# Kernel tuning notes

Measured on AMD Instinct MI355X. Metric: run time of the kernel, lower is better.

## Reference

```python
import jax, jax.numpy as jnp
import numpy as np

N_NODES = 50000
N_EDGES = 800000
D = 256
N_LAYERS = 2


def setup_inputs() -> dict:
    key = jax.random.key(0)
    k1, k2, k3, k4, k5, k6 = jax.random.split(key, 6)
    inp = {}
    inp["input"] = jax.random.normal(k1, (N_NODES, D), dtype=jnp.float32)
    inp["edge_index"] = jax.random.randint(k2, (2, N_EDGES), 0, N_NODES, dtype=jnp.int64)
    # learned params: initial dense projection + per-conv GCN weights
    scale = 1.0 / np.sqrt(D)
    inp["weight"] = jax.random.normal(k3, (D, D), dtype=jnp.float32) * scale
    inp["bias"] = jnp.zeros((D,), dtype=jnp.float32)
    inp["conv_w"] = jax.random.normal(k4, (N_LAYERS, D, D), dtype=jnp.float32) * scale
    inp["conv_b"] = jnp.zeros((N_LAYERS, D), dtype=jnp.float32)
    return inp


def _gcn_conv(x, W, b, src, dst, n):
    # Standard GCNConv: x' = D^{-1/2} (A + I) D^{-1/2} (x W) + b
    h = x @ W  # [N, D]
    loops = jnp.arange(n, dtype=src.dtype)
    s = jnp.concatenate([src, loops])
    d = jnp.concatenate([dst, loops])
    deg = jax.ops.segment_sum(jnp.ones(s.shape[0], dtype=x.dtype), d, num_segments=n)
    dinv = jnp.where(deg > 0, deg ** -0.5, 0.0)
    norm = dinv[s] * dinv[d]  # [E+N]
    msg = h[s] * norm[:, None]  # gather + scale  [E+N, D]
    return jax.ops.segment_sum(msg, d, num_segments=n) + b  # scatter-add


def reference(input, edge_index, weight, bias, conv_w, conv_b):
    n = input.shape[0]
    src, dst = edge_index[0], edge_index[1]
    # dropout=0 / eval mode -> identity
    x = jax.nn.relu(input @ weight + bias)
    for i in range(conv_w.shape[0]):
        x = jax.nn.relu(_gcn_conv(x, conv_w[i], conv_b[i], src, dst, n))
    return x
```

## Files before the change

### kernel.cpp

```cpp
#include <hip/hip_runtime.h>

#define D 256
typedef unsigned short u16;
typedef __attribute__((ext_vector_type(8))) short bf16x8;
typedef __attribute__((ext_vector_type(4))) float f32x4;

__device__ __forceinline__ float bf2f(u16 u) {
    union { unsigned int i; float f; } x; x.i = ((unsigned int)u) << 16; return x.f;
}
__device__ __forceinline__ u16 f2bf(float f) {
    union { float f; unsigned int i; } x; x.f = f;
    unsigned int r = x.i + 0x7fff + ((x.i >> 16) & 1);
    return (u16)(r >> 16);
}
__device__ __forceinline__ void gload16(const void* g, void* l) {
    __builtin_amdgcn_global_load_lds(
        (const __attribute__((address_space(1))) void*)g,
        (__attribute__((address_space(3))) void*)l, 16, 0, 0);
}


__global__ void init_kernel(int* __restrict__ deg, int* __restrict__ cursor, int n) {
    int i = blockIdx.x * blockDim.x + threadIdx.x;
    if (i < n) { deg[i] = 1; cursor[i] = 0; }
}

__global__ void hist_kernel(const int* __restrict__ dst, int* __restrict__ deg, int e) {
    int i = blockIdx.x * blockDim.x + threadIdx.x;
    int b = i * 4;
    if (b + 3 < e) {
        int4 v = *reinterpret_cast<const int4*>(&dst[b]);
        atomicAdd(&deg[v.x], 1); atomicAdd(&deg[v.y], 1);
        atomicAdd(&deg[v.z], 1); atomicAdd(&deg[v.w], 1);
    } else {
        for (int j = b; j < e; ++j) atomicAdd(&deg[dst[j]], 1);
    }
}

__global__ void dinv_kernel(const int* __restrict__ deg, float* __restrict__ dinv, int n) {
    int i = blockIdx.x * blockDim.x + threadIdx.x;
    if (i < n) dinv[i] = rsqrtf((float)deg[i]);
}


__global__ __launch_bounds__(256) void scan_phase1(
    const int* __restrict__ deg, int* __restrict__ bsum, int n) {
    __shared__ int red[256];
    int t = threadIdx.x;
    int i0 = blockIdx.x * 1024 + t * 4;
    int s = 0;
    if (i0 + 3 < n) {
        int4 v = *reinterpret_cast<const int4*>(&deg[i0]);
        s = v.x + v.y + v.z + v.w - 4;
    } else {
        for (int j = i0; j < n && j < i0 + 4; ++j) s += deg[j] - 1;
    }
    red[t] = s;
    __syncthreads();
    for (int off = 128; off > 0; off >>= 1) {
        if (t < off) red[t] += red[t + off];
        __syncthreads();
    }
    if (t == 0) bsum[blockIdx.x] = red[0];
}

__global__ __launch_bounds__(256) void scan_phase2(
    const int* __restrict__ bsum, int* __restrict__ boff,
    int* __restrict__ rowptr, int nblk, int n) {
    __shared__ int sums[256];
    int t = threadIdx.x;
    int v = (t < nblk) ? bsum[t] : 0;
    int orig = v;
    sums[t] = v;
    __syncthreads();
    for (int off = 1; off < 256; off <<= 1) {
        int u = (t >= off) ? sums[t - off] : 0;
        __syncthreads();
        sums[t] += u;
        __syncthreads();
    }
    if (t < nblk) boff[t] = sums[t] - orig;
    if (t == nblk - 1) rowptr[n] = sums[t];
}

__global__ __launch_bounds__(256) void scan_phase3(
    const int* __restrict__ deg, const int* __restrict__ boff,
    int* __restrict__ rowptr, int n) {
    __shared__ int sums[256];
    int t = threadIdx.x;
    int i0 = blockIdx.x * 1024 + t * 4;
    int d0 = 0, d1 = 0, d2 = 0, d3 = 0;
    if (i0 + 3 < n) {
        int4 v = *reinterpret_cast<const int4*>(&deg[i0]);
        d0 = v.x - 1; d1 = v.y - 1; d2 = v.z - 1; d3 = v.w - 1;
    } else {
        if (i0 + 0 < n) d0 = deg[i0 + 0] - 1;
        if (i0 + 1 < n) d1 = deg[i0 + 1] - 1;
        if (i0 + 2 < n) d2 = deg[i0 + 2] - 1;
        if (i0 + 3 < n) d3 = deg[i0 + 3] - 1;
    }
    int ts = d0 + d1 + d2 + d3;
    sums[t] = ts;
    __syncthreads();
    for (int off = 1; off < 256; off <<= 1) {
        int u = (t >= off) ? sums[t - off] : 0;
        __syncthreads();
        sums[t] += u;
        __syncthreads();
    }
    int pre = boff[blockIdx.x] + sums[t] - ts;
    if (i0 + 0 < n) rowptr[i0 + 0] = pre; pre += d0;
    if (i0 + 1 < n) rowptr[i0 + 1] = pre; pre += d1;
    if (i0 + 2 < n) rowptr[i0 + 2] = pre; pre += d2;
    if (i0 + 3 < n) rowptr[i0 + 3] = pre;
}

__global__ void fill_kernel(const int* __restrict__ src, const int* __restrict__ dst,
                            const int* __restrict__ rowptr, int* __restrict__ cursor,
                            int* __restrict__ csr, int e) {
    int i = blockIdx.x * blockDim.x + threadIdx.x;
    if (i < e) {
        int d = dst[i];
        int p = atomicAdd(&cursor[d], 1);
        csr[rowptr[d] + p] = src[i];
    }
}


__global__ void cvt_kernel(const float* __restrict__ in, u16* __restrict__ out, int n4) {
    int i = blockIdx.x * blockDim.x + threadIdx.x;
    if (i < n4) {
        float4 v = *reinterpret_cast<const float4*>(&in[(size_t)i * 4]);
        ushort4 o;
        o.x = f2bf(v.x); o.y = f2bf(v.y); o.z = f2bf(v.z); o.w = f2bf(v.w);
        *reinterpret_cast<ushort4*>(&out[(size_t)i * 4]) = o;
    }
}

__global__ __launch_bounds__(256) void transpose_cvt_kernel(
    const float* __restrict__ W, u16* __restrict__ Wt) {
    __shared__ float t[32][33];
    int bx = blockIdx.x * 32, by = blockIdx.y * 32;
    int tx = threadIdx.x & 31, ty = threadIdx.x >> 5;
#pragma unroll
    for (int i = 0; i < 32; i += 8)
        t[ty + i][tx] = W[(size_t)(bx + ty + i) * D + by + tx];
    __syncthreads();
#pragma unroll
    for (int i = 0; i < 32; i += 8)
        Wt[(size_t)(by + ty + i) * D + bx + tx] = f2bf(t[tx][ty + i]);
}

__global__ __launch_bounds__(256) void mfma_gemm(
    const u16* __restrict__ A, const u16* __restrict__ Bt,
    const float* __restrict__ bias, const float* __restrict__ dinv,
    u16* __restrict__ C, int M, int mode)
{
    __shared__ u16 As[128 * 32];
    __shared__ u16 Bs[128 * 32];
    const int tid = threadIdx.x;
    const int lane = tid & 63;
    const int wave = tid >> 6;
    const int wr = wave >> 1, wc = wave & 1;
    const int row0 = blockIdx.y * 128, col0 = blockIdx.x * 128;
    const int l16 = lane & 15, kg = lane >> 4;

    f32x4 acc[4][4] = {};

    for (int k0 = 0; k0 < D; k0 += 32) {
#pragma unroll
        for (int i = 0; i < 2; ++i) {
            int idx = i * 256 + tid;
            int r = idx >> 2, c = idx & 3;
            int csw = c ^ ((r >> 1) & 3);
            char* ldsbase_a = (char*)As + ((i * 256 + (tid & ~63)) << 4);
            char* ldsbase_b = (char*)Bs + ((i * 256 + (tid & ~63)) << 4);
            int grow = row0 + r; if (grow >= M) grow = M - 1;
            gload16(&A[(size_t)grow * D + k0 + csw * 8], ldsbase_a);
            gload16(&Bt[(size_t)(col0 + r) * D + k0 + csw * 8], ldsbase_b);
        }
        __syncthreads();
        bf16x8 af[4], bfr[4];
        int ksw = kg ^ ((l16 >> 1) & 3);
#pragma unroll
        for (int m = 0; m < 4; ++m) {
            int row = wr * 64 + m * 16 + l16;
            af[m] = *reinterpret_cast<const bf16x8*>(&As[row * 32 + ksw * 8]);
        }
#pragma unroll
        for (int nn = 0; nn < 4; ++nn) {
            int row = wc * 64 + nn * 16 + l16;
            bfr[nn] = *reinterpret_cast<const bf16x8*>(&Bs[row * 32 + ksw * 8]);
        }
#pragma unroll
        for (int m = 0; m < 4; ++m)
#pragma unroll
            for (int nn = 0; nn < 4; ++nn)
                acc[m][nn] = __builtin_amdgcn_mfma_f32_16x16x32_bf16(
                    af[m], bfr[nn], acc[m][nn], 0, 0, 0);
        __syncthreads();
    }

#pragma unroll
    for (int m = 0; m < 4; ++m) {
#pragma unroll
        for (int nn = 0; nn < 4; ++nn) {
            int gcol = col0 + wc * 64 + nn * 16 + l16;
#pragma unroll
            for (int j = 0; j < 4; ++j) {
                int grow = row0 + wr * 64 + m * 16 + kg * 4 + j;
                if (grow >= M) continue;
                float v = acc[m][nn][j];
                if (mode == 0) v = fmaxf(v + bias[gcol], 0.f);
                else           v *= dinv[grow];
                C[(size_t)grow * D + gcol] = f2bf(v);
            }
        }
    }
}

__global__ __launch_bounds__(256) void agg_kernel(
    const u16* __restrict__ hn, const int* __restrict__ rowptr,
    const int* __restrict__ csr, const float* __restrict__ dinv,
    const float* __restrict__ bias,
    u16* __restrict__ out_bf, float* __restrict__ out_f32, int n)
{
    int wave = threadIdx.x >> 6;
    int lane = threadIdx.x & 63;
    int node = blockIdx.x * 4 + wave;
    if (node >= n) return;
    int h = lane >> 5;
    int l5 = lane & 31;
    int c8 = l5 * 8;

    float a[8] = {0.f, 0.f, 0.f, 0.f, 0.f, 0.f, 0.f, 0.f};

#define ACC8(vv) { \
    a[0] += bf2f((u16)(vv)[0]); a[1] += bf2f((u16)(vv)[1]); \
    a[2] += bf2f((u16)(vv)[2]); a[3] += bf2f((u16)(vv)[3]); \
    a[4] += bf2f((u16)(vv)[4]); a[5] += bf2f((u16)(vv)[5]); \
    a[6] += bf2f((u16)(vv)[6]); a[7] += bf2f((u16)(vv)[7]); }

    if (h == 0) {
        bf16x8 v = *reinterpret_cast<const bf16x8*>(&hn[(size_t)node * D + c8]);
        ACC8(v);
    }

    int e0 = rowptr[node], e1 = rowptr[node + 1];
    for (int base = e0; base < e1; base += 64) {
        int bi = base + lane;
        int idx = (bi < e1) ? csr[bi] : 0;
        int cnt = e1 - base; if (cnt > 64) cnt = 64;
        int it = 0;
        for (; it + 8 <= cnt; it += 8) {
            int s0 = __shfl(idx, it + 0 + h);
            int s1 = __shfl(idx, it + 2 + h);
            int s2 = __shfl(idx, it + 4 + h);
            int s3 = __shfl(idx, it + 6 + h);
            bf16x8 v0 = *reinterpret_cast<const bf16x8*>(&hn[(size_t)s0 * D + c8]);
            bf16x8 v1 = *reinterpret_cast<const bf16x8*>(&hn[(size_t)s1 * D + c8]);
            bf16x8 v2 = *reinterpret_cast<const bf16x8*>(&hn[(size_t)s2 * D + c8]);
            bf16x8 v3 = *reinterpret_cast<const bf16x8*>(&hn[(size_t)s3 * D + c8]);
            ACC8(v0); ACC8(v1); ACC8(v2); ACC8(v3);
        }
        for (; it + 2 <= cnt; it += 2) {
            int s0 = __shfl(idx, it + h);
            bf16x8 v0 = *reinterpret_cast<const bf16x8*>(&hn[(size_t)s0 * D + c8]);
            ACC8(v0);
        }
        if (it < cnt) {
            int s0 = __shfl(idx, it);
            if (h == 0) {
                bf16x8 v0 = *reinterpret_cast<const bf16x8*>(&hn[(size_t)s0 * D + c8]);
                ACC8(v0);
            }
        }
    }
#undef ACC8

#pragma unroll
    for (int j = 0; j < 8; ++j) a[j] += __shfl(a[j], lane ^ 32);

    if (h == 0) {
        float di = dinv[node];
#pragma unroll
        for (int j = 0; j < 8; ++j) a[j] = fmaxf(a[j] * di + bias[c8 + j], 0.f);
        if (out_bf) {
            bf16x8 o;
#pragma unroll
            for (int j = 0; j < 8; ++j) o[j] = (short)f2bf(a[j]);
            *reinterpret_cast<bf16x8*>(&out_bf[(size_t)node * D + c8]) = o;
        } else {
            float4 o0, o1;
            o0.x = a[0]; o0.y = a[1]; o0.z = a[2]; o0.w = a[3];
            o1.x = a[4]; o1.y = a[5]; o1.z = a[6]; o1.w = a[7];
            *reinterpret_cast<float4*>(&out_f32[(size_t)node * D + c8 + 0]) = o0;
            *reinterpret_cast<float4*>(&out_f32[(size_t)node * D + c8 + 4]) = o1;
        }
    }
}


extern "C" void kernel_launch(void* const* d_in, const int* in_sizes, int n_in,
                              void* d_out, int out_size, void* d_ws, size_t ws_size,
                              hipStream_t stream) {
    const float* input  = (const float*)d_in[0];
    const int*   edge   = (const int*)d_in[1];
    const float* weight = (const float*)d_in[2];
    const float* bias   = (const float*)d_in[3];
    const float* conv_w = (const float*)d_in[4];
    const float* conv_b = (const float*)d_in[5];
    float* out = (float*)d_out;

    const int n = in_sizes[0] / D;
    const int E = in_sizes[1] / 2;
    const int* src = edge;
    const int* dst = edge + E;

    char* ws = (char*)d_ws;
    size_t off = 0;
    auto alloc = [&](size_t bytes) -> void* {
        void* p = ws + off;
        off = (off + bytes + 255) & ~(size_t)255;
        return p;
    };
    u16*   Ain    = (u16*)alloc((size_t)n * D * sizeof(u16));
    u16*   bufA   = (u16*)alloc((size_t)n * D * sizeof(u16));
    u16*   bufB   = (u16*)alloc((size_t)n * D * sizeof(u16));
    u16*   Wt     = (u16*)alloc((size_t)3 * D * D * sizeof(u16));
    int*   deg    = (int*)alloc((size_t)n * sizeof(int));
    int*   cursor = (int*)alloc((size_t)n * sizeof(int));
    float* dinv   = (float*)alloc((size_t)n * sizeof(float));
    int*   rowptr = (int*)alloc((size_t)(n + 1) * sizeof(int));
    int*   csr    = (int*)alloc((size_t)E * sizeof(int));
    int    nscan  = (n + 1023) / 1024;
    int*   bsum   = (int*)alloc((size_t)nscan * sizeof(int));
    int*   boff   = (int*)alloc((size_t)nscan * sizeof(int));

    int nb = (n + 255) / 256;
    int eb = (E + 255) / 256;
    int eb4 = (E / 4 + 255) / 256;
    init_kernel<<<nb, 256, 0, stream>>>(deg, cursor, n);
    hist_kernel<<<eb4, 256, 0, stream>>>(dst, deg, E);
    dinv_kernel<<<nb, 256, 0, stream>>>(deg, dinv, n);
    scan_phase1<<<nscan, 256, 0, stream>>>(deg, bsum, n);
    scan_phase2<<<1, 256, 0, stream>>>(bsum, boff, rowptr, nscan, n);
    scan_phase3<<<nscan, 256, 0, stream>>>(deg, boff, rowptr, n);
    fill_kernel<<<eb, 256, 0, stream>>>(src, dst, rowptr, cursor, csr, E);

    int n4 = n * D / 4;
    cvt_kernel<<<(n4 + 255) / 256, 256, 0, stream>>>(input, Ain, n4);
    dim3 tgrid(8, 8);
    transpose_cvt_kernel<<<tgrid, 256, 0, stream>>>(weight, Wt);
    transpose_cvt_kernel<<<tgrid, 256, 0, stream>>>(conv_w, Wt + D * D);
    transpose_cvt_kernel<<<tgrid, 256, 0, stream>>>(conv_w + D * D, Wt + 2 * D * D);

    dim3 ggrid(D / 128, (n + 127) / 128);
    mfma_gemm<<<ggrid, 256, 0, stream>>>(Ain, Wt, bias, dinv, bufA, n, 0);
    mfma_gemm<<<ggrid, 256, 0, stream>>>(bufA, Wt + D * D, nullptr, dinv, bufB, n, 1);
    agg_kernel<<<(n + 3) / 4, 256, 0, stream>>>(bufB, rowptr, csr, dinv, conv_b, bufA, nullptr, n);
    mfma_gemm<<<ggrid, 256, 0, stream>>>(bufA, Wt + 2 * D * D, nullptr, dinv, bufB, n, 1);
    agg_kernel<<<(n + 3) / 4, 256, 0, stream>>>(bufB, rowptr, csr, dinv, conv_b + D, nullptr, out, n);
}
```

Baseline: 343.7 us.

## Fuse input fp32-to-bf16 conversion into first GEMM, merge dinv into scan, vectorize fill

The separate fp32-to-bf16 conversion pass over the input is removed. The first GEMM now loads fp32 rows directly, converts them with a packed bf16 instruction, and writes them to LDS, which avoids an extra round trip through global memory. The dinv computation moves into the first scan phase, the CSR fill handles four edges per thread, and the aggregation loop gets a 16-wide unrolled gather to keep more loads in flight. The trade-off is that the first GEMM's A tile loads become synchronous register loads instead of direct global-to-LDS transfers, and the fused GEMM carries a leftover empty loop.

Result: faster. 329.9 us (-4.0%).

```diff
diff --git a/kernel.cpp b/kernel.cpp
--- a/kernel.cpp
+++ b/kernel.cpp
@@ -12,6 +12,11 @@
     union { float f; unsigned int i; } x; x.f = f;
     unsigned int r = x.i + 0x7fff + ((x.i >> 16) & 1);
     return (u16)(r >> 16);
+}
+__device__ __forceinline__ unsigned int cvtpk_bf16(float lo, float hi) {
+    unsigned int r;
+    asm("v_cvt_pk_bf16_f32 %0, %1, %2" : "=v"(r) : "v"(lo), "v"(hi));
+    return r;
 }
 __device__ __forceinline__ void gload16(const void* g, void* l) {
     __builtin_amdgcn_global_load_lds(
@@ -37,14 +42,10 @@
     }
 }
 
-__global__ void dinv_kernel(const int* __restrict__ deg, float* __restrict__ dinv, int n) {
-    int i = blockIdx.x * blockDim.x + threadIdx.x;
-    if (i < n) dinv[i] = rsqrtf((float)deg[i]);
-}
-
 
 __global__ __launch_bounds__(256) void scan_phase1(
-    const int* __restrict__ deg, int* __restrict__ bsum, int n) {
+    const int* __restrict__ deg, int* __restrict__ bsum,
+    float* __restrict__ dinv, int n) {
     __shared__ int red[256];
     int t = threadIdx.x;
     int i0 = blockIdx.x * 1024 + t * 4;
@@ -52,8 +53,15 @@
     if (i0 + 3 < n) {
         int4 v = *reinterpret_cast<const int4*>(&deg[i0]);
         s = v.x + v.y + v.z + v.w - 4;
+        float4 dv;
+        dv.x = rsqrtf((float)v.x); dv.y = rsqrtf((float)v.y);
+        dv.z = rsqrtf((float)v.z); dv.w = rsqrtf((float)v.w);
+        *reinterpret_cast<float4*>(&dinv[i0]) = dv;
     } else {
-        for (int j = i0; j < n && j < i0 + 4; ++j) s += deg[j] - 1;
+        for (int j = i0; j < n && j < i0 + 4; ++j) {
+            s += deg[j] - 1;
+            dinv[j] = rsqrtf((float)deg[j]);
+        }
     }
     red[t] = s;
     __syncthreads();
@@ -119,23 +127,24 @@
                             const int* __restrict__ rowptr, int* __restrict__ cursor,
                             int* __restrict__ csr, int e) {
     int i = blockIdx.x * blockDim.x + threadIdx.x;
-    if (i < e) {
-        int d = dst[i];
-        int p = atomicAdd(&cursor[d], 1);
-        csr[rowptr[d] + p] = src[i];
-    }
-}
-
-
-__global__ void cvt_kernel(const float* __restrict__ in, u16* __restrict__ out, int n4) {
-    int i = blockIdx.x * blockDim.x + threadIdx.x;
-    if (i < n4) {
-        float4 v = *reinterpret_cast<const float4*>(&in[(size_t)i * 4]);
-        ushort4 o;
-        o.x = f2bf(v.x); o.y = f2bf(v.y); o.z = f2bf(v.z); o.w = f2bf(v.w);
-        *reinterpret_cast<ushort4*>(&out[(size_t)i * 4]) = o;
-    }
-}
+    int b = i * 4;
+    if (b + 3 < e) {
+        int4 s4 = *reinterpret_cast<const int4*>(&src[b]);
+        int4 d4 = *reinterpret_cast<const int4*>(&dst[b]);
+        int p;
+        p = atomicAdd(&cursor[d4.x], 1); csr[rowptr[d4.x] + p] = s4.x;
+        p = atomicAdd(&cursor[d4.y], 1); csr[rowptr[d4.y] + p] = s4.y;
+        p = atomicAdd(&cursor[d4.z], 1); csr[rowptr[d4.z] + p] = s4.z;
+        p = atomicAdd(&cursor[d4.w], 1); csr[rowptr[d4.w] + p] = s4.w;
+    } else {
+        for (int j = b; j < e; ++j) {
+            int d = dst[j];
+            int p = atomicAdd(&cursor[d], 1);
+            csr[rowptr[d] + p] = src[j];
+        }
+    }
+}
+
 
 __global__ __launch_bounds__(256) void transpose_cvt_kernel(
     const float* __restrict__ W, u16* __restrict__ Wt) {
@@ -151,10 +160,11 @@
         Wt[(size_t)(by + ty + i) * D + bx + tx] = f2bf(t[tx][ty + i]);
 }
 
+
 __global__ __launch_bounds__(256) void mfma_gemm(
     const u16* __restrict__ A, const u16* __restrict__ Bt,
-    const float* __restrict__ bias, const float* __restrict__ dinv,
-    u16* __restrict__ C, int M, int mode)
+    const float* __restrict__ dinv,
+    u16* __restrict__ C, int M)
 {
     __shared__ u16 As[128 * 32];
     __shared__ u16 Bs[128 * 32];
@@ -183,15 +193,11 @@
         bf16x8 af[4], bfr[4];
         int ksw = kg ^ ((l16 >> 1) & 3);
 #pragma unroll
-        for (int m = 0; m < 4; ++m) {
-            int row = wr * 64 + m * 16 + l16;
-            af[m] = *reinterpret_cast<const bf16x8*>(&As[row * 32 + ksw * 8]);
-        }
-#pragma unroll
-        for (int nn = 0; nn < 4; ++nn) {
-            int row = wc * 64 + nn * 16 + l16;
-            bfr[nn] = *reinterpret_cast<const bf16x8*>(&Bs[row * 32 + ksw * 8]);
-        }
+        for (int m = 0; m < 4; ++m)
+            af[m] = *reinterpret_cast<const bf16x8*>(&As[(wr * 64 + m * 16 + l16) * 32 + ksw * 8]);
+#pragma unroll
+        for (int nn = 0; nn < 4; ++nn)
+            bfr[nn] = *reinterpret_cast<const bf16x8*>(&Bs[(wc * 64 + nn * 16 + l16) * 32 + ksw * 8]);
 #pragma unroll
         for (int m = 0; m < 4; ++m)
 #pragma unroll
@@ -210,10 +216,86 @@
             for (int j = 0; j < 4; ++j) {
                 int grow = row0 + wr * 64 + m * 16 + kg * 4 + j;
                 if (grow >= M) continue;
-                float v = acc[m][nn][j];
-                if (mode == 0) v = fmaxf(v + bias[gcol], 0.f);
-                else           v *= dinv[grow];
-                C[(size_t)grow * D + gcol] = f2bf(v);
+                C[(size_t)grow * D + gcol] = f2bf(acc[m][nn][j] * dinv[grow]);
+            }
+        }
+    }
+}
+
+__global__ __launch_bounds__(256) void mfma_gemm_f32a(
+    const float* __restrict__ A, const u16* __restrict__ Bt,
+    const float* __restrict__ bias,
+    u16* __restrict__ C, int M)
+{
+    __shared__ u16 As[128 * 32];
+    __shared__ u16 Bs[128 * 32];
+    const int tid = threadIdx.x;
+    const int lane = tid & 63;
+    const int wave = tid >> 6;
+    const int wr = wave >> 1, wc = wave & 1;
+    const int row0 = blockIdx.y * 128, col0 = blockIdx.x * 128;
+    const int l16 = lane & 15, kg = lane >> 4;
+
+    f32x4 acc[4][4] = {};
+
+    for (int k0 = 0; k0 < D; k0 += 32) {
+#pragma unroll
+        for (int i = 0; i < 2; ++i) {
+            int idx = i * 256 + tid;
+            int r = idx >> 2, c = idx & 3;
+            int csw = c ^ ((r >> 1) & 3);
+            char* ldsbase_b = (char*)Bs + ((i * 256 + (tid & ~63)) << 4);
+            gload16(&Bt[(size_t)(col0 + r) * D + k0 + csw * 8], ldsbase_b);
+        }
+#pragma unroll
+        for (int i = 0; i < 4; ++i) {
+            int idx = i * 256 + tid;
+            int r = idx >> 3, c = idx & 7;
+        }
+#pragma unroll
+        for (int i = 0; i < 2; ++i) {
+            int idx = i * 256 + tid;
+            int r = idx >> 2, c = idx & 3;
+            int csw = c ^ ((r >> 1) & 3);
+            int grow = row0 + r; if (grow >= M) grow = M - 1;
+            const float* gp = &A[(size_t)grow * D + k0 + csw * 8];
+            float4 v0 = *reinterpret_cast<const float4*>(gp);
+            float4 v1 = *reinterpret_cast<const float4*>(gp + 4);
+            uint4 w;
+            w.x = cvtpk_bf16(v0.x, v0.y);
+            w.y = cvtpk_bf16(v0.z, v0.w);
+            w.z = cvtpk_bf16(v1.x, v1.y);
+            w.w = cvtpk_bf16(v1.z, v1.w);
+            *reinterpret_cast<uint4*>((char*)As + (idx << 4)) = w;
+        }
+        __syncthreads();
+        bf16x8 af[4], bfr[4];
+        int ksw = kg ^ ((l16 >> 1) & 3);
+#pragma unroll
+        for (int m = 0; m < 4; ++m)
+            af[m] = *reinterpret_cast<const bf16x8*>(&As[(wr * 64 + m * 16 + l16) * 32 + ksw * 8]);
+#pragma unroll
+        for (int nn = 0; nn < 4; ++nn)
+            bfr[nn] = *reinterpret_cast<const bf16x8*>(&Bs[(wc * 64 + nn * 16 + l16) * 32 + ksw * 8]);
+#pragma unroll
+        for (int m = 0; m < 4; ++m)
+#pragma unroll
+            for (int nn = 0; nn < 4; ++nn)
+                acc[m][nn] = __builtin_amdgcn_mfma_f32_16x16x32_bf16(
+                    af[m], bfr[nn], acc[m][nn], 0, 0, 0);
+        __syncthreads();
+    }
+
+#pragma unroll
+    for (int m = 0; m < 4; ++m) {
+#pragma unroll
+        for (int nn = 0; nn < 4; ++nn) {
+            int gcol = col0 + wc * 64 + nn * 16 + l16;
+#pragma unroll
+            for (int j = 0; j < 4; ++j) {
+                int grow = row0 + wr * 64 + m * 16 + kg * 4 + j;
+                if (grow >= M) continue;
+                C[(size_t)grow * D + gcol] = f2bf(fmaxf(acc[m][nn][j] + bias[gcol], 0.f));
             }
         }
     }
@@ -240,11 +322,9 @@
     a[2] += bf2f((u16)(vv)[2]); a[3] += bf2f((u16)(vv)[3]); \
     a[4] += bf2f((u16)(vv)[4]); a[5] += bf2f((u16)(vv)[5]); \
     a[6] += bf2f((u16)(vv)[6]); a[7] += bf2f((u16)(vv)[7]); }
-
-    if (h == 0) {
-        bf16x8 v = *reinterpret_cast<const bf16x8*>(&hn[(size_t)node * D + c8]);
-        ACC8(v);
-    }
+#define LOADROW(s) (*reinterpret_cast<const bf16x8*>(&hn[(size_t)(s) * D + c8]))
+
+    if (h == 0) { bf16x8 v = LOADROW(node); ACC8(v); }
 
     int e0 = rowptr[node], e1 = rowptr[node + 1];
     for (int base = e0; base < e1; base += 64) {
@@ -252,31 +332,43 @@
         int idx = (bi < e1) ? csr[bi] : 0;
         int cnt = e1 - base; if (cnt > 64) cnt = 64;
         int it = 0;
+        for (; it + 16 <= cnt; it += 16) {
+            int s0 = __shfl(idx, it + 0  + h);
+            int s1 = __shfl(idx, it + 2  + h);
+            int s2 = __shfl(idx, it + 4  + h);
+            int s3 = __shfl(idx, it + 6  + h);
+            int s4 = __shfl(idx, it + 8  + h);
+            int s5 = __shfl(idx, it + 10 + h);
+            int s6 = __shfl(idx, it + 12 + h);
+            int s7 = __shfl(idx, it + 14 + h);
+            bf16x8 v0 = LOADROW(s0); bf16x8 v1 = LOADROW(s1);
+            bf16x8 v2 = LOADROW(s2); bf16x8 v3 = LOADROW(s3);
+            bf16x8 v4 = LOADROW(s4); bf16x8 v5 = LOADROW(s5);
+            bf16x8 v6 = LOADROW(s6); bf16x8 v7 = LOADROW(s7);
+            ACC8(v0); ACC8(v1); ACC8(v2); ACC8(v3);
+            ACC8(v4); ACC8(v5); ACC8(v6); ACC8(v7);
+        }
         for (; it + 8 <= cnt; it += 8) {
             int s0 = __shfl(idx, it + 0 + h);
             int s1 = __shfl(idx, it + 2 + h);
             int s2 = __shfl(idx, it + 4 + h);
             int s3 = __shfl(idx, it + 6 + h);
-            bf16x8 v0 = *reinterpret_cast<const bf16x8*>(&hn[(size_t)s0 * D + c8]);
-            bf16x8 v1 = *reinterpret_cast<const bf16x8*>(&hn[(size_t)s1 * D + c8]);
-            bf16x8 v2 = *reinterpret_cast<const bf16x8*>(&hn[(size_t)s2 * D + c8]);
-            bf16x8 v3 = *reinterpret_cast<const bf16x8*>(&hn[(size_t)s3 * D + c8]);
+            bf16x8 v0 = LOADROW(s0); bf16x8 v1 = LOADROW(s1);
+            bf16x8 v2 = LOADROW(s2); bf16x8 v3 = LOADROW(s3);
             ACC8(v0); ACC8(v1); ACC8(v2); ACC8(v3);
         }
         for (; it + 2 <= cnt; it += 2) {
             int s0 = __shfl(idx, it + h);
-            bf16x8 v0 = *reinterpret_cast<const bf16x8*>(&hn[(size_t)s0 * D + c8]);
+            bf16x8 v0 = LOADROW(s0);
             ACC8(v0);
         }
         if (it < cnt) {
             int s0 = __shfl(idx, it);
-            if (h == 0) {
-                bf16x8 v0 = *reinterpret_cast<const bf16x8*>(&hn[(size_t)s0 * D + c8]);
-                ACC8(v0);
-            }
+            if (h == 0) { bf16x8 v0 = LOADROW(s0); ACC8(v0); }
         }
     }
 #undef ACC8
+#undef LOADROW
 
 #pragma unroll
     for (int j = 0; j < 8; ++j) a[j] += __shfl(a[j], lane ^ 32);
@@ -324,7 +416,6 @@
         off = (off + bytes + 255) & ~(size_t)255;
         return p;
     };
-    u16*   Ain    = (u16*)alloc((size_t)n * D * sizeof(u16));
     u16*   bufA   = (u16*)alloc((size_t)n * D * sizeof(u16));
     u16*   bufB   = (u16*)alloc((size_t)n * D * sizeof(u16));
     u16*   Wt     = (u16*)alloc((size_t)3 * D * D * sizeof(u16));
@@ -338,27 +429,23 @@
     int*   boff   = (int*)alloc((size_t)nscan * sizeof(int));
 
     int nb = (n + 255) / 256;
-    int eb = (E + 255) / 256;
     int eb4 = (E / 4 + 255) / 256;
     init_kernel<<<nb, 256, 0, stream>>>(deg, cursor, n);
     hist_kernel<<<eb4, 256, 0, stream>>>(dst, deg, E);
-    dinv_kernel<<<nb, 256, 0, stream>>>(deg, dinv, n);
-    scan_phase1<<<nscan, 256, 0, stream>>>(deg, bsum, n);
+    scan_phase1<<<nscan, 256, 0, stream>>>(deg, bsum, dinv, n);
     scan_phase2<<<1, 256, 0, stream>>>(bsum, boff, rowptr, nscan, n);
     scan_phase3<<<nscan, 256, 0, stream>>>(deg, boff, rowptr, n);
-    fill_kernel<<<eb, 256, 0, stream>>>(src, dst, rowptr, cursor, csr, E);
-
-    int n4 = n * D / 4;
-    cvt_kernel<<<(n4 + 255) / 256, 256, 0, stream>>>(input, Ain, n4);
+    fill_kernel<<<eb4, 256, 0, stream>>>(src, dst, rowptr, cursor, csr, E);
+
     dim3 tgrid(8, 8);
     transpose_cvt_kernel<<<tgrid, 256, 0, stream>>>(weight, Wt);
     transpose_cvt_kernel<<<tgrid, 256, 0, stream>>>(conv_w, Wt + D * D);
     transpose_cvt_kernel<<<tgrid, 256, 0, stream>>>(conv_w + D * D, Wt + 2 * D * D);
 
     dim3 ggrid(D / 128, (n + 127) / 128);
-    mfma_gemm<<<ggrid, 256, 0, stream>>>(Ain, Wt, bias, dinv, bufA, n, 0);
-    mfma_gemm<<<ggrid, 256, 0, stream>>>(bufA, Wt + D * D, nullptr, dinv, bufB, n, 1);
+    mfma_gemm_f32a<<<ggrid, 256, 0, stream>>>(input, Wt, bias, bufA, n);
+    mfma_gemm<<<ggrid, 256, 0, stream>>>(bufA, Wt + D * D, dinv, bufB, n);
     agg_kernel<<<(n + 3) / 4, 256, 0, stream>>>(bufB, rowptr, csr, dinv, conv_b, bufA, nullptr, n);
-    mfma_gemm<<<ggrid, 256, 0, stream>>>(bufA, Wt + 2 * D * D, nullptr, dinv, bufB, n, 1);
+    mfma_gemm<<<ggrid, 256, 0, stream>>>(bufA, Wt + 2 * D * D, dinv, bufB, n);
     agg_kernel<<<(n + 3) / 4, 256, 0, stream>>>(bufB, rowptr, csr, dinv, conv_b + D, nullptr, out, n);
 }
```
